# Performance work log

Measured on AMD Instinct MI355X. Metric: run time of the kernel, lower is better.

Reference implementation:

```python
import math
import jax, jax.numpy as jnp
import numpy as np

N_HEADS = 16
D_EMBED = 1024
D_HEAD = D_EMBED // N_HEADS


def setup_inputs() -> dict:
    key = jax.random.key(0)
    k1, k2, k3, k4, k5 = jax.random.split(key, 5)
    B, S, D = 4, 2048, D_EMBED
    scale = 1.0 / math.sqrt(D)
    return {
        "x": jax.random.normal(k1, (B, S, D), dtype=jnp.float32),
        "in_proj_w": jax.random.normal(k2, (3 * D, D), dtype=jnp.float32) * scale,
        "in_proj_b": jax.random.normal(k3, (3 * D,), dtype=jnp.float32) * 0.02,
        "out_proj_w": jax.random.normal(k4, (D, D), dtype=jnp.float32) * scale,
        "out_proj_b": jax.random.normal(k5, (D,), dtype=jnp.float32) * 0.02,
        "causal_mask": 0,
    }


def reference(x, in_proj_w, in_proj_b, out_proj_w, out_proj_b, causal_mask):
    B, S, D = x.shape
    # in_proj: torch Linear -> x @ W^T + b, then chunk into q,k,v
    qkv = x @ in_proj_w.T + in_proj_b              # [B,S,3D]
    q, k, v = jnp.split(qkv, 3, axis=-1)
    # [B,S,D] -> [B,H,S,d]
    def heads(t):
        return t.reshape(B, S, N_HEADS, D_HEAD).transpose(0, 2, 1, 3)
    q, k, v = heads(q), heads(k), heads(v)
    weight = jnp.einsum("bhsd,bhtd->bhst", q, k)   # [B,H,S,S] materialized scores
    if causal_mask:
        mask = jnp.triu(jnp.ones((S, S), dtype=bool), k=1)
        weight = jnp.where(mask, -jnp.inf, weight)
    weight = jax.nn.softmax(weight / math.sqrt(D_HEAD), axis=-1)
    out = jnp.einsum("bhst,bhtd->bhsd", weight, v)  # [B,H,S,d]
    out = out.transpose(0, 2, 1, 3).reshape(B, S, D)
    return out @ out_proj_w.T + out_proj_b
```

## Files before the change

### kernel.cpp

```cpp
#include <hip/hip_runtime.h>

typedef unsigned short u16;
typedef _Float16 h8 __attribute__((ext_vector_type(8)));
typedef __fp16 fp16x2 __attribute__((ext_vector_type(2)));
typedef float f32x4 __attribute__((ext_vector_type(4)));

constexpr int B_ = 4, S_ = 2048, D_ = 1024, H_ = 16;

__device__ __forceinline__ void async16(const void* g, void* l) {
  __builtin_amdgcn_global_load_lds(
      (const __attribute__((address_space(1))) void*)g,
      (__attribute__((address_space(3))) void*)l, 16, 0, 0);
}

__device__ __forceinline__ unsigned pk2(float a, float b) {
  union { fp16x2 h; unsigned u; } c;
  c.h = __builtin_amdgcn_cvt_pkrtz(a, b);
  return c.u;
}

__global__ __launch_bounds__(256) void cvt3_kernel(
    const float* __restrict__ x, const float* __restrict__ wi,
    const float* __restrict__ wo, _Float16* __restrict__ xh,
    _Float16* __restrict__ wih, _Float16* __restrict__ woh)
{
  const int bid = blockIdx.x;
  const float* src;
  _Float16* dst;
  int base;
  if (bid < 8192)       { src = x;  dst = xh;  base = bid; }
  else if (bid < 11264) { src = wi; dst = wih; base = bid - 8192; }
  else                  { src = wo; dst = woh; base = bid - 11264; }
  const int i = (base * 256 + threadIdx.x) * 4;
  const float4 v = *(const float4*)(src + i);
  uint2 o;
  o.x = pk2(v.x, v.y);
  o.y = pk2(v.z, v.w);
  *(uint2*)(dst + i) = o;
}

template<bool OUT_HALF, int BPW>
__global__ __launch_bounds__(512, 2) void gemm256d_f16(
    const _Float16* __restrict__ A, const _Float16* __restrict__ Bw,
    const float* __restrict__ bias, void* __restrict__ Cout,
    int M, int N, int K)
{
  constexpr int BN = BPW * 64;
  constexpr int NBB = BN / 8;
  __shared__ __align__(16) _Float16 sA[2][16384];
  __shared__ __align__(16) _Float16 sB[2][NBB * 512];

  const int tid = threadIdx.x;
  const int lane = tid & 63, w = tid >> 6;
  const int wm = w >> 2, wn = w & 3;

  const int id = blockIdx.x;
  const int cpx = gridDim.x >> 3;
  const int swz = (id & 7) * cpx + (id >> 3);
  const int nbx = N / BN;
  const int bx = swz % nbx, by = swz / nbx;
  const int m0 = by * 256, n0 = bx * BN;

  const int r15 = lane & 15, s4 = lane >> 4;
  const _Float16* gA[4];
  int loA[4];
#pragma unroll
  for (int j = 0; j < 4; ++j) {
    const int t = 2 * w + (j >> 1), kk = j & 1;
    gA[j] = A + (size_t)(m0 + 16 * t + r15) * K + kk * 32 + s4 * 8;
    loA[j] = (t * 2 + kk) * 512;
  }
  const _Float16* gB[BPW];
  int loB[BPW];
#pragma unroll
  for (int j = 0; j < BPW; ++j) {
    const int f = w * BPW + j, nt = f >> 1, kk = f & 1;
    gB[j] = Bw + (size_t)(n0 + 16 * nt + r15) * K + kk * 32 + s4 * 8;
    loB[j] = f * 512;
  }

  const f32x4 zf = {0.f, 0.f, 0.f, 0.f};
  f32x4 acc[8][BPW];
#pragma unroll
  for (int i = 0; i < 8; ++i)
#pragma unroll
    for (int j = 0; j < BPW; ++j) acc[i][j] = zf;

#pragma unroll
  for (int j = 0; j < 4; ++j) async16(gA[j], &sA[0][loA[j]]);
#pragma unroll
  for (int j = 0; j < BPW; ++j) async16(gB[j], &sB[0][loB[j]]);
#pragma unroll
  for (int j = 0; j < 4; ++j) async16(gA[j] + 64, &sA[1][loA[j]]);
#pragma unroll
  for (int j = 0; j < BPW; ++j) async16(gB[j] + 64, &sB[1][loB[j]]);
  if constexpr (BPW == 4) asm volatile("s_waitcnt vmcnt(8)" ::: "memory");
  else                    asm volatile("s_waitcnt vmcnt(7)" ::: "memory");
  __builtin_amdgcn_s_barrier();

  const int NT = K >> 6;
  int cur = 0;
  for (int kt = 0; kt < NT; ++kt) {
    const _Float16* pA = sA[cur];
    const _Float16* pB = sB[cur];
    _Float16* nA = sA[cur];
    _Float16* nB = sB[cur];
    const bool st = (kt + 2 < NT);
    const int ko = (kt + 2) * 64;

    h8 fb[BPW][2];
#pragma unroll
    for (int p = 0; p < 4; ++p) {
      if (p == 0) {
#pragma unroll
        for (int nt = 0; nt < BPW; ++nt)
#pragma unroll
          for (int kk = 0; kk < 2; ++kk)
            fb[nt][kk] = *(const h8*)&pB[((wn * BPW + nt) * 2 + kk) * 512 + lane * 8];
      } else if (st) {
        if (p == 1) {
#pragma unroll
          for (int j = 0; j < BPW; ++j) async16(gB[j] + ko, &nB[loB[j]]);
        }
        if ((w & 3) == p - 1) {
#pragma unroll
          for (int j = 0; j < 4; ++j) async16(gA[j] + ko, &nA[loA[j]]);
        }
      }
      h8 fa[2][2];
#pragma unroll
      for (int i = 0; i < 2; ++i)
#pragma unroll
        for (int kk = 0; kk < 2; ++kk)
          fa[i][kk] = *(const h8*)&pA[((wm * 8 + 2 * p + i) * 2 + kk) * 512 + lane * 8];
      __builtin_amdgcn_s_setprio(1);
#pragma unroll
      for (int i = 0; i < 2; ++i)
#pragma unroll
        for (int nt = 0; nt < BPW; ++nt)
#pragma unroll
          for (int kk = 0; kk < 2; ++kk)
            acc[2 * p + i][nt] = __builtin_amdgcn_mfma_f32_16x16x32_f16(
                fa[i][kk], fb[nt][kk], acc[2 * p + i][nt], 0, 0, 0);
      __builtin_amdgcn_s_setprio(0);
      __builtin_amdgcn_s_barrier();
    }
    if (st && (w & 3) == 3) {
#pragma unroll
      for (int j = 0; j < 4; ++j) async16(gA[j] + ko, &nA[loA[j]]);
    }
    if (kt + 1 < NT) {
      if (st) {
        if constexpr (BPW == 4) asm volatile("s_waitcnt vmcnt(8)" ::: "memory");
        else                    asm volatile("s_waitcnt vmcnt(7)" ::: "memory");
      } else {
        asm volatile("s_waitcnt vmcnt(0)" ::: "memory");
      }
      __builtin_amdgcn_s_barrier();
    }
    cur ^= 1;
  }

  const int g = lane >> 4, cc = lane & 15;
#pragma unroll
  for (int nt = 0; nt < BPW; ++nt) {
    const int col = n0 + wn * (16 * BPW) + nt * 16 + cc;
    const float bv = bias[col];
#pragma unroll
    for (int mt = 0; mt < 8; ++mt) {
      const int rowb = m0 + wm * 128 + mt * 16 + g * 4;
#pragma unroll
      for (int r = 0; r < 4; ++r) {
        const float v = acc[mt][nt][r] + bv;
        if constexpr (OUT_HALF)
          ((_Float16*)Cout)[(size_t)(rowb + r) * N + col] = (_Float16)v;
        else
          ((float*)Cout)[(size_t)(rowb + r) * N + col] = v;
      }
    }
  }
}

template<bool OUT_HALF>
__global__ __launch_bounds__(256) void gemm_f16(
    const _Float16* __restrict__ A, const _Float16* __restrict__ Bw,
    const float* __restrict__ bias, void* __restrict__ Cout,
    int M, int N, int K)
{
  __shared__ __align__(16) _Float16 sA[4096];
  __shared__ __align__(16) _Float16 sB[4096];

  const int tid = threadIdx.x;
  const int lane = tid & 63, w = tid >> 6;
  const int wm = w & 1, wn = w >> 1;
  const int m0 = blockIdx.y * 128, n0 = blockIdx.x * 128;

  const int sr = 16 * w + (lane & 15);
  const int ss = lane >> 4;
  const _Float16* gA1 = A + (size_t)(m0 + sr) * K + 8 * ss;
  const _Float16* gA2 = gA1 + (size_t)64 * K;
  const _Float16* gB1 = Bw + (size_t)(n0 + sr) * K + 8 * ss;
  const _Float16* gB2 = gB1 + (size_t)64 * K;
  _Float16* lA1 = &sA[w * 512];
  _Float16* lA2 = &sA[(w + 4) * 512];
  _Float16* lB1 = &sB[w * 512];
  _Float16* lB2 = &sB[(w + 4) * 512];

  const f32x4 zf = {0.f, 0.f, 0.f, 0.f};
  f32x4 acc[4][4];
#pragma unroll
  for (int i = 0; i < 4; ++i)
#pragma unroll
    for (int j = 0; j < 4; ++j) acc[i][j] = zf;

  for (int k0 = 0; k0 < K; k0 += 32) {
    __syncthreads();
    async16(gA1 + k0, lA1);
    async16(gA2 + k0, lA2);
    async16(gB1 + k0, lB1);
    async16(gB2 + k0, lB2);
    __syncthreads();

    h8 fa[4], fb[4];
#pragma unroll
    for (int i = 0; i < 4; ++i) {
      fa[i] = *(const h8*)&sA[((wm * 4 + i) << 9) + (lane << 3)];
      fb[i] = *(const h8*)&sB[((wn * 4 + i) << 9) + (lane << 3)];
    }
#pragma unroll
    for (int i = 0; i < 4; ++i)
#pragma unroll
      for (int j = 0; j < 4; ++j)
        acc[i][j] = __builtin_amdgcn_mfma_f32_16x16x32_f16(fa[i], fb[j], acc[i][j], 0, 0, 0);
  }

  const int g = lane >> 4, cc = lane & 15;
#pragma unroll
  for (int j = 0; j < 4; ++j) {
    const int col = n0 + (wn * 4 + j) * 16 + cc;
    const float bv = bias[col];
#pragma unroll
    for (int i = 0; i < 4; ++i) {
      const int rowb = m0 + (wm * 4 + i) * 16 + g * 4;
#pragma unroll
      for (int r = 0; r < 4; ++r) {
        const float v = acc[i][j][r] + bv;
        if constexpr (OUT_HALF)
          ((_Float16*)Cout)[(size_t)(rowb + r) * N + col] = (_Float16)v;
        else
          ((float*)Cout)[(size_t)(rowb + r) * N + col] = v;
      }
    }
  }
}

__global__ __launch_bounds__(256) void transpose_v(
    const u16* __restrict__ qkv, u16* __restrict__ vT)
{
  __shared__ u16 T[64 * 73];
  const int tid = threadIdx.x;
  const int bh = blockIdx.y, s0 = blockIdx.x * 64;
  const int b = bh >> 4, h = bh & 15;
#pragma unroll
  for (int t = 0; t < 2; ++t) {
    const int c = tid + t * 256, r = c >> 3, cs = c & 7;
    union { int4 v; u16 s[8]; } u;
    u.v = *(const int4*)(qkv + (size_t)(b * S_ + s0 + r) * 3072 + 2048 + h * 64 + 8 * cs);
#pragma unroll
    for (int i = 0; i < 8; ++i) T[r * 73 + 8 * cs + i] = u.s[i];
  }
  __syncthreads();
#pragma unroll
  for (int t = 0; t < 2; ++t) {
    const int c = tid + t * 256, rd = c >> 3, ss = c & 7;
    union { int4 v; u16 s[8]; } u;
#pragma unroll
    for (int i = 0; i < 8; ++i) u.s[i] = T[(8 * ss + i) * 73 + rd];
    *(int4*)(vT + (size_t)(bh * 64 + rd) * S_ + s0 + 8 * ss) = u.v;
  }
}

__global__ __launch_bounds__(256, 4) void attn_f16(
    const _Float16* __restrict__ qkv, const _Float16* __restrict__ vT,
    _Float16* __restrict__ attnO, const int* __restrict__ causal_ptr)
{
  __shared__ __align__(16) _Float16 sQP[9216];
  __shared__ __align__(16) _Float16 sK[4096];
  __shared__ __align__(16) _Float16 sV[4096];

  const int tid = threadIdx.x, lane = tid & 63, w = tid >> 6;
  const int q4 = lane >> 4, cc = lane & 15;
  const int bh = blockIdx.y, b = bh >> 4, h = bh & 15;
  const int q0 = blockIdx.x * 128;
  const int causal = causal_ptr[0];

  {
    const int rr = lane & 15, sc8 = lane >> 4;
#pragma unroll
    for (int tt = 0; tt < 2; ++tt) {
      const int t = 2 * w + tt;
#pragma unroll
      for (int sh = 0; sh < 2; ++sh) {
        const _Float16* g = qkv + (size_t)(b * S_ + q0 + 16 * t + rr) * 3072 + h * 64 + 8 * (4 * sh + sc8);
        async16(g, &sQP[t * 1024 + sh * 512]);
      }
    }
  }
  __syncthreads();

  h8 qf[2][2];
#pragma unroll
  for (int m = 0; m < 2; ++m)
#pragma unroll
    for (int kk = 0; kk < 2; ++kk) {
      h8 v = *(const h8*)&sQP[((2 * w + m) << 10) + (kk << 9) + (lane << 3)];
      qf[m][kk] = v * (_Float16)0.125f;
    }

  h8 ones;
#pragma unroll
  for (int i = 0; i < 8; ++i) ones[i] = (_Float16)1.0f;

  const _Float16* gK = qkv + (size_t)(b * S_ + 16 * w + (lane & 15)) * 3072 + 1024 + h * 64 + 8 * (lane >> 4);
  const _Float16* gV = vT + (size_t)(bh * 64 + 16 * w + (lane & 15)) * S_ + 8 * (lane >> 4);
  _Float16* lK0 = &sK[w * 1024];
  _Float16* lV0 = &sV[w * 1024];

  const int wp = w * 2304;

  const f32x4 zf = {0.f, 0.f, 0.f, 0.f};
  f32x4 oa[2][4], lac[2];
#pragma unroll
  for (int m = 0; m < 2; ++m) {
    lac[m] = zf;
#pragma unroll
    for (int nt = 0; nt < 4; ++nt) oa[m][nt] = zf;
  }

  for (int j0 = 0; j0 < S_; j0 += 64) {
    if (causal && j0 > q0 + 127) break;
    __syncthreads();
    async16(gK + (size_t)j0 * 3072, lK0);
    async16(gK + (size_t)j0 * 3072 + 32, lK0 + 512);
    async16(gV + j0, lV0);
    async16(gV + j0 + 32, lV0 + 512);
    __syncthreads();

    f32x4 sc[2][4];
#pragma unroll
    for (int nt = 0; nt < 4; ++nt) {
      const h8 kf0 = *(const h8*)&sK[(nt << 10) + (lane << 3)];
      const h8 kf1 = *(const h8*)&sK[(nt << 10) + 512 + (lane << 3)];
#pragma unroll
      for (int m = 0; m < 2; ++m) {
        sc[m][nt] = __builtin_amdgcn_mfma_f32_16x16x32_f16(kf0, qf[m][0], zf, 0, 0, 0);
        sc[m][nt] = __builtin_amdgcn_mfma_f32_16x16x32_f16(kf1, qf[m][1], sc[m][nt], 0, 0, 0);
      }
    }

    if (causal) {
#pragma unroll
      for (int m = 0; m < 2; ++m)
#pragma unroll
        for (int nt = 0; nt < 4; ++nt)
#pragma unroll
          for (int r = 0; r < 4; ++r)
            if ((j0 + nt * 16 + q4 * 4 + r) > (q0 + 32 * w + m * 16 + cc))
              sc[m][nt][r] = -1.0e30f;
    }

#pragma unroll
    for (int m = 0; m < 2; ++m)
#pragma unroll
      for (int nt = 0; nt < 4; ++nt) {
        uint2 pk;
        pk.x = pk2(__expf(sc[m][nt][0]), __expf(sc[m][nt][1]));
        pk.y = pk2(__expf(sc[m][nt][2]), __expf(sc[m][nt][3]));
        *(uint2*)&sQP[wp + (m * 16 + cc) * 72 + nt * 16 + q4 * 4] = pk;
      }

    asm volatile("s_waitcnt lgkmcnt(0)" ::: "memory");

    h8 pf[2][2];
#pragma unroll
    for (int m = 0; m < 2; ++m)
#pragma unroll
      for (int kk = 0; kk < 2; ++kk)
        pf[m][kk] = *(const h8*)&sQP[wp + (m * 16 + cc) * 72 + kk * 32 + q4 * 8];

#pragma unroll
    for (int m = 0; m < 2; ++m) {
      lac[m] = __builtin_amdgcn_mfma_f32_16x16x32_f16(pf[m][0], ones, lac[m], 0, 0, 0);
      lac[m] = __builtin_amdgcn_mfma_f32_16x16x32_f16(pf[m][1], ones, lac[m], 0, 0, 0);
    }
#pragma unroll
    for (int nt = 0; nt < 4; ++nt) {
      const h8 vf0 = *(const h8*)&sV[(nt << 10) + (lane << 3)];
      const h8 vf1 = *(const h8*)&sV[(nt << 10) + 512 + (lane << 3)];
#pragma unroll
      for (int m = 0; m < 2; ++m) {
        oa[m][nt] = __builtin_amdgcn_mfma_f32_16x16x32_f16(pf[m][0], vf0, oa[m][nt], 0, 0, 0);
        oa[m][nt] = __builtin_amdgcn_mfma_f32_16x16x32_f16(pf[m][1], vf1, oa[m][nt], 0, 0, 0);
      }
    }
  }

#pragma unroll
  for (int m = 0; m < 2; ++m) {
    float inv[4];
#pragma unroll
    for (int r = 0; r < 4; ++r) inv[r] = 1.0f / lac[m][r];
#pragma unroll
    for (int nt = 0; nt < 4; ++nt) {
      const int col = h * 64 + nt * 16 + cc;
#pragma unroll
      for (int r = 0; r < 4; ++r) {
        const int row = b * S_ + q0 + 32 * w + m * 16 + q4 * 4 + r;
        attnO[(size_t)row * D_ + col] = (_Float16)(oa[m][nt][r] * inv[r]);
      }
    }
  }
}

extern "C" void kernel_launch(void* const* d_in, const int* in_sizes, int n_in,
                              void* d_out, int out_size, void* d_ws, size_t ws_size,
                              hipStream_t stream)
{
  const float* x  = (const float*)d_in[0];
  const float* wi = (const float*)d_in[1];
  const float* bi = (const float*)d_in[2];
  const float* wo = (const float*)d_in[3];
  const float* bo = (const float*)d_in[4];
  const int* causal = (const int*)d_in[5];

  _Float16* xh   = (_Float16*)d_ws;
  _Float16* wih  = xh + 8388608;
  _Float16* woh  = wih + 3145728;
  _Float16* qkvb = woh + 1048576;
  _Float16* vT   = qkvb + 25165824;
  _Float16* attn = vT + 8388608;

  const int M = B_ * S_;

  cvt3_kernel<<<12288, 256, 0, stream>>>(x, wi, wo, xh, wih, woh);

  gemm256d_f16<true, 3><<<512, 512, 0, stream>>>(
      xh, wih, bi, qkvb, M, 3 * D_, D_);

  transpose_v<<<dim3(32, 64), 256, 0, stream>>>((const u16*)qkvb, (u16*)vT);

  attn_f16<<<dim3(16, 64), 256, 0, stream>>>(qkvb, vT, attn, causal);

  gemm_f16<false><<<dim3(8, 64), 256, 0, stream>>>(
      attn, woh, bo, d_out, M, D_, D_);
}
```

Baseline: 311.1 us.

## Fuse V transpose and Q scaling into QKV GEMM epilogue; use exp2 in attention

The QKV projection GEMM epilogue now writes V columns directly in transposed layout into the vT buffer, which removes the separate transpose_v kernel and its extra read and write pass over V. Q columns are pre-scaled by 1/sqrt(d)*log2(e) so attention can use the native exp2 instead of __expf and skip the per-fragment Q multiply. Attention blocks are launched on a 1D swizzled grid so neighbouring blocks share K/V in cache, and MFMA phases are wrapped in s_setprio. The trade-off is that the transposed V stores are narrow 8-byte scattered writes, and Q now carries the scale in fp16 rounding.

New measurement: 294.6 us. 1.06x faster.

```diff
diff --git a/kernel.cpp b/kernel.cpp
--- a/kernel.cpp
+++ b/kernel.cpp
@@ -18,6 +18,16 @@
   c.h = __builtin_amdgcn_cvt_pkrtz(a, b);
   return c.u;
 }
+
+__device__ __forceinline__ float fexp2(float x) {
+#if __has_builtin(__builtin_amdgcn_exp2f)
+  return __builtin_amdgcn_exp2f(x);
+#else
+  return exp2f(x);
+#endif
+}
+
+#define QSCALE 0.18033688011112042f
 
 __global__ __launch_bounds__(256) void cvt3_kernel(
     const float* __restrict__ x, const float* __restrict__ wi,
@@ -39,10 +49,11 @@
   *(uint2*)(dst + i) = o;
 }
 
-template<bool OUT_HALF, int BPW>
+template<bool OUT_HALF, int BPW, bool SCALE_Q, bool FUSE_V>
 __global__ __launch_bounds__(512, 2) void gemm256d_f16(
     const _Float16* __restrict__ A, const _Float16* __restrict__ Bw,
     const float* __restrict__ bias, void* __restrict__ Cout,
+    _Float16* __restrict__ vTout,
     int M, int N, int K)
 {
   constexpr int BN = BPW * 64;
@@ -94,8 +105,9 @@
   for (int j = 0; j < 4; ++j) async16(gA[j] + 64, &sA[1][loA[j]]);
 #pragma unroll
   for (int j = 0; j < BPW; ++j) async16(gB[j] + 64, &sB[1][loB[j]]);
-  if constexpr (BPW == 4) asm volatile("s_waitcnt vmcnt(8)" ::: "memory");
-  else                    asm volatile("s_waitcnt vmcnt(7)" ::: "memory");
+  if constexpr (BPW == 2)      asm volatile("s_waitcnt vmcnt(6)" ::: "memory");
+  else if constexpr (BPW == 3) asm volatile("s_waitcnt vmcnt(7)" ::: "memory");
+  else                         asm volatile("s_waitcnt vmcnt(8)" ::: "memory");
   __builtin_amdgcn_s_barrier();
 
   const int NT = K >> 6;
@@ -151,8 +163,9 @@
     }
     if (kt + 1 < NT) {
       if (st) {
-        if constexpr (BPW == 4) asm volatile("s_waitcnt vmcnt(8)" ::: "memory");
-        else                    asm volatile("s_waitcnt vmcnt(7)" ::: "memory");
+        if constexpr (BPW == 2)      asm volatile("s_waitcnt vmcnt(6)" ::: "memory");
+        else if constexpr (BPW == 3) asm volatile("s_waitcnt vmcnt(7)" ::: "memory");
+        else                         asm volatile("s_waitcnt vmcnt(8)" ::: "memory");
       } else {
         asm volatile("s_waitcnt vmcnt(0)" ::: "memory");
       }
@@ -166,16 +179,32 @@
   for (int nt = 0; nt < BPW; ++nt) {
     const int col = n0 + wn * (16 * BPW) + nt * 16 + cc;
     const float bv = bias[col];
+    float qs = 1.0f;
+    if constexpr (SCALE_Q) qs = (col < 1024) ? QSCALE : 1.0f;
 #pragma unroll
     for (int mt = 0; mt < 8; ++mt) {
       const int rowb = m0 + wm * 128 + mt * 16 + g * 4;
+      float vv[4];
 #pragma unroll
       for (int r = 0; r < 4; ++r) {
-        const float v = acc[mt][nt][r] + bv;
-        if constexpr (OUT_HALF)
-          ((_Float16*)Cout)[(size_t)(rowb + r) * N + col] = (_Float16)v;
-        else
-          ((float*)Cout)[(size_t)(rowb + r) * N + col] = v;
+        vv[r] = acc[mt][nt][r] + bv;
+        if constexpr (SCALE_Q) vv[r] *= qs;
+      }
+      bool vcol = false;
+      if constexpr (FUSE_V) vcol = (col >= 2048);
+      if (vcol) {
+        union { _Float16 hx[4]; uint2 u; } pv;
+#pragma unroll
+        for (int r = 0; r < 4; ++r) pv.hx[r] = (_Float16)vv[r];
+        *(uint2*)&vTout[((size_t)(((rowb >> 11) << 10) + (col - 2048)) << 11) + (rowb & 2047)] = pv.u;
+      } else {
+#pragma unroll
+        for (int r = 0; r < 4; ++r) {
+          if constexpr (OUT_HALF)
+            ((_Float16*)Cout)[(size_t)(rowb + r) * N + col] = (_Float16)vv[r];
+          else
+            ((float*)Cout)[(size_t)(rowb + r) * N + col] = vv[r];
+        }
       }
     }
   }
@@ -254,32 +283,6 @@
   }
 }
 
-__global__ __launch_bounds__(256) void transpose_v(
-    const u16* __restrict__ qkv, u16* __restrict__ vT)
-{
-  __shared__ u16 T[64 * 73];
-  const int tid = threadIdx.x;
-  const int bh = blockIdx.y, s0 = blockIdx.x * 64;
-  const int b = bh >> 4, h = bh & 15;
-#pragma unroll
-  for (int t = 0; t < 2; ++t) {
-    const int c = tid + t * 256, r = c >> 3, cs = c & 7;
-    union { int4 v; u16 s[8]; } u;
-    u.v = *(const int4*)(qkv + (size_t)(b * S_ + s0 + r) * 3072 + 2048 + h * 64 + 8 * cs);
-#pragma unroll
-    for (int i = 0; i < 8; ++i) T[r * 73 + 8 * cs + i] = u.s[i];
-  }
-  __syncthreads();
-#pragma unroll
-  for (int t = 0; t < 2; ++t) {
-    const int c = tid + t * 256, rd = c >> 3, ss = c & 7;
-    union { int4 v; u16 s[8]; } u;
-#pragma unroll
-    for (int i = 0; i < 8; ++i) u.s[i] = T[(8 * ss + i) * 73 + rd];
-    *(int4*)(vT + (size_t)(bh * 64 + rd) * S_ + s0 + 8 * ss) = u.v;
-  }
-}
-
 __global__ __launch_bounds__(256, 4) void attn_f16(
     const _Float16* __restrict__ qkv, const _Float16* __restrict__ vT,
     _Float16* __restrict__ attnO, const int* __restrict__ causal_ptr)
@@ -290,8 +293,10 @@
 
   const int tid = threadIdx.x, lane = tid & 63, w = tid >> 6;
   const int q4 = lane >> 4, cc = lane & 15;
-  const int bh = blockIdx.y, b = bh >> 4, h = bh & 15;
-  const int q0 = blockIdx.x * 128;
+  const int id = blockIdx.x;
+  const int swz = (id & 7) * 128 + (id >> 3);
+  const int bh = swz >> 4, b = bh >> 4, h = bh & 15;
+  const int q0 = (swz & 15) << 7;
   const int causal = causal_ptr[0];
 
   {
@@ -312,10 +317,8 @@
 #pragma unroll
   for (int m = 0; m < 2; ++m)
 #pragma unroll
-    for (int kk = 0; kk < 2; ++kk) {
-      h8 v = *(const h8*)&sQP[((2 * w + m) << 10) + (kk << 9) + (lane << 3)];
-      qf[m][kk] = v * (_Float16)0.125f;
-    }
+    for (int kk = 0; kk < 2; ++kk)
+      qf[m][kk] = *(const h8*)&sQP[((2 * w + m) << 10) + (kk << 9) + (lane << 3)];
 
   h8 ones;
 #pragma unroll
@@ -347,6 +350,7 @@
     __syncthreads();
 
     f32x4 sc[2][4];
+    __builtin_amdgcn_s_setprio(1);
 #pragma unroll
     for (int nt = 0; nt < 4; ++nt) {
       const h8 kf0 = *(const h8*)&sK[(nt << 10) + (lane << 3)];
@@ -357,6 +361,7 @@
         sc[m][nt] = __builtin_amdgcn_mfma_f32_16x16x32_f16(kf1, qf[m][1], sc[m][nt], 0, 0, 0);
       }
     }
+    __builtin_amdgcn_s_setprio(0);
 
     if (causal) {
 #pragma unroll
@@ -374,8 +379,8 @@
 #pragma unroll
       for (int nt = 0; nt < 4; ++nt) {
         uint2 pk;
-        pk.x = pk2(__expf(sc[m][nt][0]), __expf(sc[m][nt][1]));
-        pk.y = pk2(__expf(sc[m][nt][2]), __expf(sc[m][nt][3]));
+        pk.x = pk2(fexp2(sc[m][nt][0]), fexp2(sc[m][nt][1]));
+        pk.y = pk2(fexp2(sc[m][nt][2]), fexp2(sc[m][nt][3]));
         *(uint2*)&sQP[wp + (m * 16 + cc) * 72 + nt * 16 + q4 * 4] = pk;
       }
 
@@ -388,6 +393,7 @@
       for (int kk = 0; kk < 2; ++kk)
         pf[m][kk] = *(const h8*)&sQP[wp + (m * 16 + cc) * 72 + kk * 32 + q4 * 8];
 
+    __builtin_amdgcn_s_setprio(1);
 #pragma unroll
     for (int m = 0; m < 2; ++m) {
       lac[m] = __builtin_amdgcn_mfma_f32_16x16x32_f16(pf[m][0], ones, lac[m], 0, 0, 0);
@@ -403,6 +409,7 @@
         oa[m][nt] = __builtin_amdgcn_mfma_f32_16x16x32_f16(pf[m][1], vf1, oa[m][nt], 0, 0, 0);
       }
     }
+    __builtin_amdgcn_s_setprio(0);
   }
 
 #pragma unroll
@@ -444,12 +451,10 @@
 
   cvt3_kernel<<<12288, 256, 0, stream>>>(x, wi, wo, xh, wih, woh);
 
-  gemm256d_f16<true, 3><<<512, 512, 0, stream>>>(
-      xh, wih, bi, qkvb, M, 3 * D_, D_);
-
-  transpose_v<<<dim3(32, 64), 256, 0, stream>>>((const u16*)qkvb, (u16*)vT);
-
-  attn_f16<<<dim3(16, 64), 256, 0, stream>>>(qkvb, vT, attn, causal);
+  gemm256d_f16<true, 3, true, true><<<512, 512, 0, stream>>>(
+      xh, wih, bi, qkvb, vT, M, 3 * D_, D_);
+
+  attn_f16<<<1024, 256, 0, stream>>>(qkvb, vT, attn, causal);
 
   gemm_f16<false><<<dim3(8, 64), 256, 0, stream>>>(
       attn, woh, bo, d_out, M, D_, D_);
```
